# Optimization experiments

Hardware: AMD Instinct MI355X
Metric: run time of the kernel (lower is better)

Reference implementation:

```python
import jax, jax.numpy as jnp
import numpy as np
from jax import lax

STEP_SIZE = 0.5  # params['step_size'] in the original


def setup_inputs() -> dict:
    key = jax.random.key(0)
    ks = jax.random.split(key, 7)
    B, D_IN, H, D_OUT = 16384, 784, 1024, 10
    return {
        "x": jax.random.normal(ks[0], (B, D_IN), dtype=jnp.float32),
        "u1": jax.random.normal(ks[1], (B, H), dtype=jnp.float32),
        "u2": jax.random.normal(ks[2], (B, D_OUT), dtype=jnp.float32),
        "W1": jax.random.normal(ks[3], (D_IN, H), dtype=jnp.float32),
        "W2": jax.random.normal(ks[4], (H, D_OUT), dtype=jnp.float32),
        "b1": jax.random.normal(ks[5], (H,), dtype=jnp.float32),
        "b2": jax.random.normal(ks[6], (D_OUT,), dtype=jnp.float32),
        "steps": 50,
    }


def reference(x, u1, u2, W1, W2, b1, b2, steps):
    """Free-phase (beta=0) settle of EquilibriumPropagationNet, batched.

    Energy: E = 0.5(|u1|^2+|u2|^2) - 0.5*x@W1@rho(u1) - rho(u1)@W2@rho(u2)
                - b1.rho(u1) - b2.rho(u2)
    Each settle step does u -= step_size * dE/du (closed form of autograd).
    Note the 0.5 factor on the x@W1 term is kept, matching the source exactly.
    """
    xW1 = x @ W1  # [B,H], constant across settle steps

    def step(carry, _):
        u1, u2 = carry
        r1 = jax.nn.sigmoid(u1)
        r2 = jax.nn.sigmoid(u2)
        d1 = r1 * (1.0 - r1)  # sigmoid'
        d2 = r2 * (1.0 - r2)
        g1 = u1 - d1 * (0.5 * xW1 + r2 @ W2.T + b1)  # dE/du1
        g2 = u2 - d2 * (r1 @ W2 + b2)                # dE/du2 (beta=0)
        return (u1 - STEP_SIZE * g1, u2 - STEP_SIZE * g2), None

    (u1, u2), _ = lax.scan(step, (u1, u2), None, length=steps)
    y_pred = jax.nn.sigmoid(u2)  # [B,10]
    return y_pred
```

## Files before the change

kernel.cpp:

```cpp
#include <hip/hip_runtime.h>
#include <hip/hip_bf16.h>
#include <stdint.h>


typedef __attribute__((ext_vector_type(8))) short bf16x8;
typedef __attribute__((ext_vector_type(4))) float f32x4;

#define D_IN  784
#define KPAD  800
#define HID   1024
#define D_OUT 10

__device__ __forceinline__ uint32_t fbits(float f){ union{float f;uint32_t u;}v; v.f=f; return v.u; }
__device__ __forceinline__ float asf(uint32_t u){ union{uint32_t u;float f;}v; v.u=u; return v.f; }
__device__ __forceinline__ unsigned short f2bf(float f){ __hip_bfloat16 h=__float2bfloat16(f); return *reinterpret_cast<unsigned short*>(&h); }
__device__ __forceinline__ uint32_t pack2(unsigned short a, unsigned short b){ return (uint32_t)a | ((uint32_t)b<<16); }
__device__ __forceinline__ float sigmoidf_(float x){ return __builtin_amdgcn_rcpf(1.0f + __expf(-x)); }
__device__ __forceinline__ uint32_t cvtpk_bf16(float a, float b){
    uint32_t d;
    asm("v_cvt_pk_bf16_f32 %0, %1, %2" : "=v"(d) : "v"(a), "v"(b));
    return d;
}

__global__ void prep_w1t(const float* __restrict__ W1,
                         unsigned short* __restrict__ w1h, unsigned short* __restrict__ w1l) {
    __shared__ float tile[32][33];
    int kt = blockIdx.x % 25;
    int nt = blockIdx.x / 25;
    int t  = threadIdx.x;
    int kk = t / 8;
    int nn = (t % 8) * 4;
    int k  = kt * 32 + kk;
    float4 v = make_float4(0.f, 0.f, 0.f, 0.f);
    if (k < D_IN)
        v = *reinterpret_cast<const float4*>(W1 + (size_t)k * HID + nt * 32 + nn);
    tile[kk][nn + 0] = v.x; tile[kk][nn + 1] = v.y;
    tile[kk][nn + 2] = v.z; tile[kk][nn + 3] = v.w;
    __syncthreads();
    int nn2 = t / 8;
    int kk2 = (t % 8) * 4;
    unsigned short hs[4], ls[4];
#pragma unroll
    for (int i = 0; i < 4; i++) {
        float f = tile[kk2 + i][nn2];
        uint32_t hb = fbits(f) & 0xffff0000u;
        hs[i] = (unsigned short)(hb >> 16);
        ls[i] = f2bf(f - asf(hb));
    }
    size_t o = (size_t)(nt * 32 + nn2) * KPAD + kt * 32 + kk2;
    uint2 hv; hv.x = pack2(hs[0], hs[1]); hv.y = pack2(hs[2], hs[3]);
    uint2 lv; lv.x = pack2(ls[0], ls[1]); lv.y = pack2(ls[2], ls[3]);
    *reinterpret_cast<uint2*>(w1h + o) = hv;
    *reinterpret_cast<uint2*>(w1l + o) = lv;
}

__global__ __launch_bounds__(256) void gemm_c1(
    const float* __restrict__ x,
    const unsigned short* __restrict__ w1h, const unsigned short* __restrict__ w1l,
    const float* __restrict__ b1, float* __restrict__ c1)
{
    __shared__ unsigned short Ah[128][40];
    __shared__ unsigned short Al[128][40];
    __shared__ unsigned short Bh[128][40];
    __shared__ unsigned short Bl[128][40];
    int bm = blockIdx.x >> 3;
    int bn = blockIdx.x & 7;
    int t = threadIdx.x;
    int lane = t & 63;
    int wid  = t >> 6;
    int r = lane & 15, g = lane >> 4;
    int wm = wid >> 1, wn = wid & 1;

    f32x4 acc[4][4];
    f32x4 zero = {0.f, 0.f, 0.f, 0.f};
#pragma unroll
    for (int i = 0; i < 4; i++)
#pragma unroll
        for (int j = 0; j < 4; j++) acc[i][j] = zero;

    int srow  = t >> 1;
    int skoff = (t & 1) * 16;
    const float* xbase = x + (size_t)(bm * 128 + srow) * D_IN;
    const unsigned short* bhp = w1h + (size_t)(bn * 128 + srow) * KPAD + skoff;
    const unsigned short* blp = w1l + (size_t)(bn * 128 + srow) * KPAD + skoff;

    for (int kt = 0; kt < KPAD / 32; kt++) {
        int k0 = kt * 32 + skoff;
        float xv[16];
        if (k0 < D_IN) {
#pragma unroll
            for (int c = 0; c < 4; c++) {
                float4 f = *reinterpret_cast<const float4*>(xbase + k0 + 4 * c);
                xv[4*c+0]=f.x; xv[4*c+1]=f.y; xv[4*c+2]=f.z; xv[4*c+3]=f.w;
            }
        } else {
#pragma unroll
            for (int i = 0; i < 16; i++) xv[i] = 0.f;
        }
        uint4 vbh0 = *reinterpret_cast<const uint4*>(bhp + kt * 32);
        uint4 vbh1 = *reinterpret_cast<const uint4*>(bhp + kt * 32 + 8);
        uint4 vbl0 = *reinterpret_cast<const uint4*>(blp + kt * 32);
        uint4 vbl1 = *reinterpret_cast<const uint4*>(blp + kt * 32 + 8);
        uint32_t hw[8], lw[8];
#pragma unroll
        for (int j = 0; j < 8; j++) {
            float f0 = xv[2*j], f1 = xv[2*j+1];
            uint32_t hb0 = fbits(f0) & 0xffff0000u;
            uint32_t hb1 = fbits(f1) & 0xffff0000u;
            hw[j] = (hb0 >> 16) | hb1;
            lw[j] = pack2(f2bf(f0 - asf(hb0)), f2bf(f1 - asf(hb1)));
        }
        __syncthreads();
        *reinterpret_cast<uint4*>(&Ah[srow][skoff])     = make_uint4(hw[0],hw[1],hw[2],hw[3]);
        *reinterpret_cast<uint4*>(&Ah[srow][skoff + 8]) = make_uint4(hw[4],hw[5],hw[6],hw[7]);
        *reinterpret_cast<uint4*>(&Al[srow][skoff])     = make_uint4(lw[0],lw[1],lw[2],lw[3]);
        *reinterpret_cast<uint4*>(&Al[srow][skoff + 8]) = make_uint4(lw[4],lw[5],lw[6],lw[7]);
        *reinterpret_cast<uint4*>(&Bh[srow][skoff])     = vbh0;
        *reinterpret_cast<uint4*>(&Bh[srow][skoff + 8]) = vbh1;
        *reinterpret_cast<uint4*>(&Bl[srow][skoff])     = vbl0;
        *reinterpret_cast<uint4*>(&Bl[srow][skoff + 8]) = vbl1;
        __syncthreads();
        bf16x8 ah[4], al[4], bh[4], bl[4];
#pragma unroll
        for (int mt = 0; mt < 4; mt++) {
            ah[mt] = *reinterpret_cast<const bf16x8*>(&Ah[wm * 64 + mt * 16 + r][g * 8]);
            al[mt] = *reinterpret_cast<const bf16x8*>(&Al[wm * 64 + mt * 16 + r][g * 8]);
        }
#pragma unroll
        for (int nt = 0; nt < 4; nt++) {
            bh[nt] = *reinterpret_cast<const bf16x8*>(&Bh[wn * 64 + nt * 16 + r][g * 8]);
            bl[nt] = *reinterpret_cast<const bf16x8*>(&Bl[wn * 64 + nt * 16 + r][g * 8]);
        }
#pragma unroll
        for (int mt = 0; mt < 4; mt++)
#pragma unroll
            for (int nt = 0; nt < 4; nt++) {
                acc[mt][nt] = __builtin_amdgcn_mfma_f32_16x16x32_bf16(ah[mt], bh[nt], acc[mt][nt], 0, 0, 0);
                acc[mt][nt] = __builtin_amdgcn_mfma_f32_16x16x32_bf16(al[mt], bh[nt], acc[mt][nt], 0, 0, 0);
                acc[mt][nt] = __builtin_amdgcn_mfma_f32_16x16x32_bf16(ah[mt], bl[nt], acc[mt][nt], 0, 0, 0);
            }
    }
#pragma unroll
    for (int nt = 0; nt < 4; nt++) {
        int n = bn * 128 + wn * 64 + nt * 16 + r;
        float bias = b1[n];
#pragma unroll
        for (int mt = 0; mt < 4; mt++) {
            int mrow = bm * 128 + wm * 64 + mt * 16 + g * 4;
#pragma unroll
            for (int q = 0; q < 4; q++)
                c1[(size_t)(mrow + q) * HID + n] = 0.5f * acc[mt][nt][q] + bias;
        }
    }
}

__global__ __launch_bounds__(1024, 4) void settle(
    const float* __restrict__ u1g, const float* __restrict__ u2g,
    const float* __restrict__ W2,  const float* __restrict__ b2,
    const float* __restrict__ c1,  const int* __restrict__ steps_ptr,
    float* __restrict__ out)
{
    __shared__ unsigned short r1hi[16][16][64];
    __shared__ unsigned short r1lo[16][16][64];
    __shared__ float s_part[16][10][20];
    __shared__ unsigned short r2p[16][40];

    int t = threadIdx.x;
    int w = t >> 6, lane = t & 63;
    int r = lane & 15, g = lane >> 4;
    int row0 = blockIdx.x * 16;
    int h0 = w * 64;

    int rr2 = t / 10, k2 = t - rr2 * 10;
    float uo = 0.f, r2o = 0.f, b2k = 0.f;
    if (t < 160) { int i = t; r2p[rr2][30 + (i % 10)] = 0; }
    if (t < 160) {
        uo = u2g[(size_t)(row0 + rr2) * D_OUT + k2];
        r2o = sigmoidf_(uo);
        b2k = b2[k2];
        uint32_t hb = fbits(r2o) & 0xffff0000u;
        unsigned short hi = (unsigned short)(hb >> 16);
        r2p[rr2][k2] = hi; r2p[rr2][k2 + 10] = hi;
        r2p[rr2][k2 + 20] = f2bf(r2o - asf(hb));
    }

    f32x4 u1f[4], c1f[4];
#pragma unroll
    for (int tt = 0; tt < 4; tt++) {
        int h = h0 + tt * 16 + 4 * g;
        u1f[tt] = *reinterpret_cast<const f32x4*>(u1g + (size_t)(row0 + r) * HID + h);
        c1f[tt] = *reinterpret_cast<const f32x4*>(c1  + (size_t)(row0 + r) * HID + h);
    }

    bf16x8 aW2[4];
#pragma unroll
    for (int tt = 0; tt < 4; tt++) {
        int h = h0 + tt * 16 + r;
#pragma unroll
        for (int j = 0; j < 8; j++) {
            int s = 8 * g + j;
            unsigned short val = 0;
            if (s < 30) {
                int k = (s < 10) ? s : (s < 20 ? s - 10 : s - 20);
                float f = W2[(size_t)h * D_OUT + k];
                uint32_t hb = fbits(f) & 0xffff0000u;
                val = (s >= 10 && s < 20) ? f2bf(f - asf(hb)) : (unsigned short)(hb >> 16);
            }
            aW2[tt][j] = (short)val;
        }
    }
    bf16x8 bWh[2], bWl[2];
#pragma unroll
    for (int kt = 0; kt < 2; kt++)
#pragma unroll
        for (int j = 0; j < 8; j++) {
            unsigned short vh = 0, vl = 0;
            if (r < D_OUT) {
                int h = h0 + kt * 32 + 8 * g + j;
                float f = W2[(size_t)h * D_OUT + r];
                uint32_t hb = fbits(f) & 0xffff0000u;
                vh = (unsigned short)(hb >> 16);
                vl = f2bf(f - asf(hb));
            }
            bWh[kt][j] = (short)vh; bWl[kt][j] = (short)vl;
        }

    const f32x4 zero = {0.f, 0.f, 0.f, 0.f};
    int steps = steps_ptr[0];

    uint2* hiw = reinterpret_cast<uint2*>(&r1hi[w][r][0]);
    uint2* low = reinterpret_cast<uint2*>(&r1lo[w][r][0]);
    const bf16x8* r2row = reinterpret_cast<const bf16x8*>(&r2p[0][0]);

    __syncthreads();

    for (int s = 0; s < steps; s++) {
        bf16x8 br2 = r2row[r * 5 + g];
#pragma unroll
        for (int tt = 0; tt < 4; tt++) {
            f32x4 m1 = __builtin_amdgcn_mfma_f32_16x16x32_bf16(aW2[tt], br2, c1f[tt], 0, 0, 0);
            f32x4 u = u1f[tt], un;
            float rv[4], lof[4];
#pragma unroll
            for (int q = 0; q < 4; q++) {
                rv[q] = sigmoidf_(u[q]);
                lof[q] = rv[q] - asf(fbits(rv[q]) & 0xffff0000u);
                float d1 = __builtin_fmaf(-rv[q], rv[q], rv[q]);
                un[q] = 0.5f * __builtin_fmaf(d1, m1[q], u[q]);
            }
            u1f[tt] = un;
            uint2 hv, lv;
            hv.x = __builtin_amdgcn_perm(fbits(rv[1]), fbits(rv[0]), 0x07060302u);
            hv.y = __builtin_amdgcn_perm(fbits(rv[3]), fbits(rv[2]), 0x07060302u);
            lv.x = cvtpk_bf16(lof[0], lof[1]);
            lv.y = cvtpk_bf16(lof[2], lof[3]);
            hiw[(4 * tt + g) ^ r] = hv;
            low[(4 * tt + g) ^ r] = lv;
        }
        f32x4 sa = zero, sb = zero;
        {
            union { uint2 p[2]; bf16x8 v; } a0, l0, a1, l1;
            a0.p[0] = hiw[(2 * g)     ^ r]; a0.p[1] = hiw[(2 * g + 1) ^ r];
            l0.p[0] = low[(2 * g)     ^ r]; l0.p[1] = low[(2 * g + 1) ^ r];
            a1.p[0] = hiw[(8 + 2 * g) ^ r]; a1.p[1] = hiw[(8 + 2 * g + 1) ^ r];
            l1.p[0] = low[(8 + 2 * g) ^ r]; l1.p[1] = low[(8 + 2 * g + 1) ^ r];
            sa = __builtin_amdgcn_mfma_f32_16x16x32_bf16(a0.v, bWh[0], sa, 0, 0, 0);
            sb = __builtin_amdgcn_mfma_f32_16x16x32_bf16(a1.v, bWh[1], sb, 0, 0, 0);
            sa = __builtin_amdgcn_mfma_f32_16x16x32_bf16(l0.v, bWh[0], sa, 0, 0, 0);
            sb = __builtin_amdgcn_mfma_f32_16x16x32_bf16(l1.v, bWh[1], sb, 0, 0, 0);
            sa = __builtin_amdgcn_mfma_f32_16x16x32_bf16(a0.v, bWl[0], sa, 0, 0, 0);
            sb = __builtin_amdgcn_mfma_f32_16x16x32_bf16(a1.v, bWl[1], sb, 0, 0, 0);
        }
        f32x4 sc = sa + sb;
        if (r < D_OUT) {
            int ws = w ^ g;
#pragma unroll
            for (int q = 0; q < 4; q++) s_part[4 * g + q][r][ws] = sc[q];
        }
        __syncthreads();
        if (t < 160) {
            const f32x4* sp = reinterpret_cast<const f32x4*>(&s_part[rr2][k2][0]);
            f32x4 v0 = sp[0], v1 = sp[1], v2 = sp[2], v3 = sp[3];
            f32x4 vs = (v0 + v1) + (v2 + v3);
            float sv = b2k + ((vs[0] + vs[1]) + (vs[2] + vs[3]));
            float d2 = __builtin_fmaf(-r2o, r2o, r2o);
            uo = 0.5f * __builtin_fmaf(d2, sv, uo);
            r2o = sigmoidf_(uo);
            uint32_t hb = fbits(r2o) & 0xffff0000u;
            unsigned short hi = (unsigned short)(hb >> 16);
            r2p[rr2][k2] = hi; r2p[rr2][k2 + 10] = hi;
            r2p[rr2][k2 + 20] = f2bf(r2o - asf(hb));
        }
        __syncthreads();
    }

    if (t < 160)
        out[(size_t)(row0 + rr2) * D_OUT + k2] = r2o;

}

extern "C" void kernel_launch(void* const* d_in, const int* in_sizes, int n_in,
                              void* d_out, int out_size, void* d_ws, size_t ws_size,
                              hipStream_t stream) {
    const float* x   = (const float*)d_in[0];
    const float* u1  = (const float*)d_in[1];
    const float* u2  = (const float*)d_in[2];
    const float* W1  = (const float*)d_in[3];
    const float* W2  = (const float*)d_in[4];
    const float* b1  = (const float*)d_in[5];
    const float* b2  = (const float*)d_in[6];
    const int* steps = (const int*)d_in[7];
    float* out = (float*)d_out;

    char* ws = (char*)d_ws;
    float* c1           = (float*)(ws);
    unsigned short* w1h = (unsigned short*)(ws + 67108864u);
    unsigned short* w1l = (unsigned short*)(ws + 67108864u + 1638400u);

    prep_w1t<<<800,  256, 0, stream>>>(W1, w1h, w1l);
    gemm_c1 <<<1024, 256, 0, stream>>>(x, w1h, w1l, b1, c1);
    settle  <<<1024, 1024, 0, stream>>>(u1, u2, W2, b2, c1, steps, out);
}
```

Baseline: 572.0 us.

## Process two 16-row groups per settle block to halve barriers per row

Each settle block now handles 32 batch rows as two independent 16-row groups, with separate r2 and partial-sum buffers for each. Both groups' u1 updates and W2 products run before a shared pair of barriers, so barrier cost per row is halved and the two groups' work can interleave. The grid is halved to 512 blocks. The cost is twice the u1/c1 register state per thread, which may raise register pressure, hurt occupancy under the 1024x4 launch bound, and leave fewer blocks to spread across CUs.

```diff
diff --git a/kernel.cpp b/kernel.cpp
--- a/kernel.cpp
+++ b/kernel.cpp
@@ -162,34 +162,42 @@
 {
     __shared__ unsigned short r1hi[16][16][64];
     __shared__ unsigned short r1lo[16][16][64];
-    __shared__ float s_part[16][10][20];
-    __shared__ unsigned short r2p[16][40];
+    __shared__ __align__(16) float s_partA[16][10][20];
+    __shared__ __align__(16) float s_partB[16][10][20];
+    __shared__ __align__(16) unsigned short r2pA[16][40];
+    __shared__ __align__(16) unsigned short r2pB[16][40];
 
     int t = threadIdx.x;
     int w = t >> 6, lane = t & 63;
     int r = lane & 15, g = lane >> 4;
-    int row0 = blockIdx.x * 16;
+    int row0 = blockIdx.x * 32;
     int h0 = w * 64;
 
-    int rr2 = t / 10, k2 = t - rr2 * 10;
+    int tg  = (t >= 160) ? 1 : 0;
+    int tb  = t - tg * 160;
+    int rr2 = tb / 10, k2 = tb - rr2 * 10;
     float uo = 0.f, r2o = 0.f, b2k = 0.f;
-    if (t < 160) { int i = t; r2p[rr2][30 + (i % 10)] = 0; }
-    if (t < 160) {
-        uo = u2g[(size_t)(row0 + rr2) * D_OUT + k2];
+    unsigned short* r2p_my = tg ? &r2pB[0][0] : &r2pA[0][0];
+    const float*    sp_my  = tg ? &s_partB[0][0][0] : &s_partA[0][0][0];
+    if (t < 320) {
+        r2p_my[rr2 * 40 + 30 + (tb % 10)] = 0;
+        uo = u2g[(size_t)(row0 + tg * 16 + rr2) * D_OUT + k2];
         r2o = sigmoidf_(uo);
         b2k = b2[k2];
         uint32_t hb = fbits(r2o) & 0xffff0000u;
         unsigned short hi = (unsigned short)(hb >> 16);
-        r2p[rr2][k2] = hi; r2p[rr2][k2 + 10] = hi;
-        r2p[rr2][k2 + 20] = f2bf(r2o - asf(hb));
-    }
-
-    f32x4 u1f[4], c1f[4];
+        r2p_my[rr2 * 40 + k2] = hi; r2p_my[rr2 * 40 + k2 + 10] = hi;
+        r2p_my[rr2 * 40 + k2 + 20] = f2bf(r2o - asf(hb));
+    }
+
+    f32x4 u1fA[4], c1fA[4], u1fB[4], c1fB[4];
 #pragma unroll
     for (int tt = 0; tt < 4; tt++) {
         int h = h0 + tt * 16 + 4 * g;
-        u1f[tt] = *reinterpret_cast<const f32x4*>(u1g + (size_t)(row0 + r) * HID + h);
-        c1f[tt] = *reinterpret_cast<const f32x4*>(c1  + (size_t)(row0 + r) * HID + h);
+        u1fA[tt] = *reinterpret_cast<const f32x4*>(u1g + (size_t)(row0 + r) * HID + h);
+        c1fA[tt] = *reinterpret_cast<const f32x4*>(c1  + (size_t)(row0 + r) * HID + h);
+        u1fB[tt] = *reinterpret_cast<const f32x4*>(u1g + (size_t)(row0 + 16 + r) * HID + h);
+        c1fB[tt] = *reinterpret_cast<const f32x4*>(c1  + (size_t)(row0 + 16 + r) * HID + h);
     }
 
     bf16x8 aW2[4];
@@ -230,56 +238,63 @@
 
     uint2* hiw = reinterpret_cast<uint2*>(&r1hi[w][r][0]);
     uint2* low = reinterpret_cast<uint2*>(&r1lo[w][r][0]);
-    const bf16x8* r2row = reinterpret_cast<const bf16x8*>(&r2p[0][0]);
+    const bf16x8* r2rowA = reinterpret_cast<const bf16x8*>(&r2pA[0][0]);
+    const bf16x8* r2rowB = reinterpret_cast<const bf16x8*>(&r2pB[0][0]);
 
     __syncthreads();
 
+#define GROUP_STEP(U1F, C1F, R2ROW, SPART)                                        \
+    {                                                                             \
+        bf16x8 br2 = R2ROW[r * 5 + g];                                            \
+        _Pragma("unroll")                                                         \
+        for (int tt = 0; tt < 4; tt++) {                                          \
+            f32x4 m1 = __builtin_amdgcn_mfma_f32_16x16x32_bf16(aW2[tt], br2, C1F[tt], 0, 0, 0); \
+            f32x4 u = U1F[tt], un;                                                \
+            float rv[4], lof[4];                                                  \
+            _Pragma("unroll")                                                     \
+            for (int q = 0; q < 4; q++) {                                         \
+                rv[q] = sigmoidf_(u[q]);                                          \
+                lof[q] = rv[q] - asf(fbits(rv[q]) & 0xffff0000u);                 \
+                float d1 = __builtin_fmaf(-rv[q], rv[q], rv[q]);                  \
+                un[q] = 0.5f * __builtin_fmaf(d1, m1[q], u[q]);                   \
+            }                                                                     \
+            U1F[tt] = un;                                                         \
+            uint2 hv, lv;                                                         \
+            hv.x = __builtin_amdgcn_perm(fbits(rv[1]), fbits(rv[0]), 0x07060302u);\
+            hv.y = __builtin_amdgcn_perm(fbits(rv[3]), fbits(rv[2]), 0x07060302u);\
+            lv.x = cvtpk_bf16(lof[0], lof[1]);                                    \
+            lv.y = cvtpk_bf16(lof[2], lof[3]);                                    \
+            hiw[(4 * tt + g) ^ r] = hv;                                           \
+            low[(4 * tt + g) ^ r] = lv;                                           \
+        }                                                                         \
+        f32x4 sa, sb;                                                             \
+        {                                                                         \
+            union { uint2 p[2]; bf16x8 v; } a0, l0, a1, l1;                       \
+            a0.p[0] = hiw[(2 * g)     ^ r]; a0.p[1] = hiw[(2 * g + 1) ^ r];       \
+            l0.p[0] = low[(2 * g)     ^ r]; l0.p[1] = low[(2 * g + 1) ^ r];       \
+            a1.p[0] = hiw[(8 + 2 * g) ^ r]; a1.p[1] = hiw[(8 + 2 * g + 1) ^ r];   \
+            l1.p[0] = low[(8 + 2 * g) ^ r]; l1.p[1] = low[(8 + 2 * g + 1) ^ r];   \
+            sa = __builtin_amdgcn_mfma_f32_16x16x32_bf16(a0.v, bWh[0], zero, 0, 0, 0); \
+            sb = __builtin_amdgcn_mfma_f32_16x16x32_bf16(a1.v, bWh[1], zero, 0, 0, 0); \
+            sa = __builtin_amdgcn_mfma_f32_16x16x32_bf16(l0.v, bWh[0], sa, 0, 0, 0);   \
+            sb = __builtin_amdgcn_mfma_f32_16x16x32_bf16(l1.v, bWh[1], sb, 0, 0, 0);   \
+            sa = __builtin_amdgcn_mfma_f32_16x16x32_bf16(a0.v, bWl[0], sa, 0, 0, 0);   \
+            sb = __builtin_amdgcn_mfma_f32_16x16x32_bf16(a1.v, bWl[1], sb, 0, 0, 0);   \
+        }                                                                         \
+        f32x4 sc = sa + sb;                                                       \
+        if (r < D_OUT) {                                                          \
+            int ws = w ^ g;                                                       \
+            _Pragma("unroll")                                                     \
+            for (int q = 0; q < 4; q++) SPART[4 * g + q][r][ws] = sc[q];          \
+        }                                                                         \
+    }
+
     for (int s = 0; s < steps; s++) {
-        bf16x8 br2 = r2row[r * 5 + g];
-#pragma unroll
-        for (int tt = 0; tt < 4; tt++) {
-            f32x4 m1 = __builtin_amdgcn_mfma_f32_16x16x32_bf16(aW2[tt], br2, c1f[tt], 0, 0, 0);
-            f32x4 u = u1f[tt], un;
-            float rv[4], lof[4];
-#pragma unroll
-            for (int q = 0; q < 4; q++) {
-                rv[q] = sigmoidf_(u[q]);
-                lof[q] = rv[q] - asf(fbits(rv[q]) & 0xffff0000u);
-                float d1 = __builtin_fmaf(-rv[q], rv[q], rv[q]);
-                un[q] = 0.5f * __builtin_fmaf(d1, m1[q], u[q]);
-            }
-            u1f[tt] = un;
-            uint2 hv, lv;
-            hv.x = __builtin_amdgcn_perm(fbits(rv[1]), fbits(rv[0]), 0x07060302u);
-            hv.y = __builtin_amdgcn_perm(fbits(rv[3]), fbits(rv[2]), 0x07060302u);
-            lv.x = cvtpk_bf16(lof[0], lof[1]);
-            lv.y = cvtpk_bf16(lof[2], lof[3]);
-            hiw[(4 * tt + g) ^ r] = hv;
-            low[(4 * tt + g) ^ r] = lv;
-        }
-        f32x4 sa = zero, sb = zero;
-        {
-            union { uint2 p[2]; bf16x8 v; } a0, l0, a1, l1;
-            a0.p[0] = hiw[(2 * g)     ^ r]; a0.p[1] = hiw[(2 * g + 1) ^ r];
-            l0.p[0] = low[(2 * g)     ^ r]; l0.p[1] = low[(2 * g + 1) ^ r];
-            a1.p[0] = hiw[(8 + 2 * g) ^ r]; a1.p[1] = hiw[(8 + 2 * g + 1) ^ r];
-            l1.p[0] = low[(8 + 2 * g) ^ r]; l1.p[1] = low[(8 + 2 * g + 1) ^ r];
-            sa = __builtin_amdgcn_mfma_f32_16x16x32_bf16(a0.v, bWh[0], sa, 0, 0, 0);
-            sb = __builtin_amdgcn_mfma_f32_16x16x32_bf16(a1.v, bWh[1], sb, 0, 0, 0);
-            sa = __builtin_amdgcn_mfma_f32_16x16x32_bf16(l0.v, bWh[0], sa, 0, 0, 0);
-            sb = __builtin_amdgcn_mfma_f32_16x16x32_bf16(l1.v, bWh[1], sb, 0, 0, 0);
-            sa = __builtin_amdgcn_mfma_f32_16x16x32_bf16(a0.v, bWl[0], sa, 0, 0, 0);
-            sb = __builtin_amdgcn_mfma_f32_16x16x32_bf16(a1.v, bWl[1], sb, 0, 0, 0);
-        }
-        f32x4 sc = sa + sb;
-        if (r < D_OUT) {
-            int ws = w ^ g;
-#pragma unroll
-            for (int q = 0; q < 4; q++) s_part[4 * g + q][r][ws] = sc[q];
-        }
+        GROUP_STEP(u1fA, c1fA, r2rowA, s_partA)
+        GROUP_STEP(u1fB, c1fB, r2rowB, s_partB)
         __syncthreads();
-        if (t < 160) {
-            const f32x4* sp = reinterpret_cast<const f32x4*>(&s_part[rr2][k2][0]);
+        if (t < 320) {
+            const f32x4* sp = reinterpret_cast<const f32x4*>(sp_my + rr2 * 200 + k2 * 20);
             f32x4 v0 = sp[0], v1 = sp[1], v2 = sp[2], v3 = sp[3];
             f32x4 vs = (v0 + v1) + (v2 + v3);
             float sv = b2k + ((vs[0] + vs[1]) + (vs[2] + vs[3]));
@@ -288,15 +303,15 @@
             r2o = sigmoidf_(uo);
             uint32_t hb = fbits(r2o) & 0xffff0000u;
             unsigned short hi = (unsigned short)(hb >> 16);
-            r2p[rr2][k2] = hi; r2p[rr2][k2 + 10] = hi;
-            r2p[rr2][k2 + 20] = f2bf(r2o - asf(hb));
+            r2p_my[rr2 * 40 + k2] = hi; r2p_my[rr2 * 40 + k2 + 10] = hi;
+            r2p_my[rr2 * 40 + k2 + 20] = f2bf(r2o - asf(hb));
         }
         __syncthreads();
     }
-
-    if (t < 160)
-        out[(size_t)(row0 + rr2) * D_OUT + k2] = r2o;
-
+#undef GROUP_STEP
+
+    if (t < 320)
+        out[(size_t)(row0 + tg * 16 + rr2) * D_OUT + k2] = r2o;
 }
 
 extern "C" void kernel_launch(void* const* d_in, const int* in_sizes, int n_in,
@@ -319,5 +334,5 @@
 
     prep_w1t<<<800,  256, 0, stream>>>(W1, w1h, w1l);
     gemm_c1 <<<1024, 256, 0, stream>>>(x, w1h, w1l, b1, c1);
-    settle  <<<1024, 1024, 0, stream>>>(u1, u2, W2, b2, c1, steps, out);
-}
+    settle  <<<512,  1024, 0, stream>>>(u1, u2, W2, b2, c1, steps, out);
+}
```

Result: slower. 1.671 ms (+192.1%).
